# Kernel optimization log

Hardware: AMD Instinct MI355X
Metric: run time of the kernel (lower is better)

The kernel has to match this reference:

```python
import jax, jax.numpy as jnp
import numpy as np

B, HW, ENC = 64, 14, 2048
T_CAP, VOCAB = 25, 10000
EMB = DEC = ATT = 512


def setup_inputs() -> dict:
    key = jax.random.key(0)
    ks = jax.random.split(key, 24)
    n = lambda k, shape, s=0.02: jax.random.normal(k, shape, jnp.float32) * s
    encoder_out = jax.random.normal(ks[0], (B, HW, HW, ENC), jnp.float32)
    captions = jax.random.randint(ks[1], (B, T_CAP), 0, VOCAB)
    lens = jax.random.randint(ks[2], (B,), 2, T_CAP + 1)
    caption_lengths = jnp.sort(lens)[::-1].at[0].set(T_CAP)  # sorted desc, max=T_CAP
    return {
        'encoder_out': encoder_out,
        'captions': captions,
        'caption_lengths': caption_lengths,
        'emb': jax.random.uniform(ks[3], (VOCAB, EMB), jnp.float32, -0.1, 0.1),
        'We_att': n(ks[4], (ENC, ATT)), 'be_att': jnp.zeros((ATT,), jnp.float32),
        'Wd_att': n(ks[5], (DEC, ATT)), 'bd_att': jnp.zeros((ATT,), jnp.float32),
        'v_att': n(ks[6], (ATT, 1)),    'bv_att': jnp.zeros((1,), jnp.float32),
        'W_ih': n(ks[7], (4 * DEC, EMB + ENC)), 'b_ih': jnp.zeros((4 * DEC,), jnp.float32),
        'W_hh': n(ks[8], (4 * DEC, DEC)),       'b_hh': jnp.zeros((4 * DEC,), jnp.float32),
        'W_init_h': n(ks[9], (ENC, DEC)),  'b_init_h': jnp.zeros((DEC,), jnp.float32),
        'W_init_c': n(ks[10], (ENC, DEC)), 'b_init_c': jnp.zeros((DEC,), jnp.float32),
        'W_fbeta': n(ks[11], (DEC, ENC)),  'b_fbeta': jnp.zeros((ENC,), jnp.float32),
        'W_fc': jax.random.uniform(ks[12], (DEC, VOCAB), jnp.float32, -0.1, 0.1),
        'b_fc': jnp.zeros((VOCAB,), jnp.float32),
    }


def reference(encoder_out, captions, caption_lengths, emb,
              We_att, be_att, Wd_att, bd_att, v_att, bv_att,
              W_ih, b_ih, W_hh, b_hh,
              W_init_h, b_init_h, W_init_c, b_init_c,
              W_fbeta, b_fbeta, W_fc, b_fc):
    Bn = encoder_out.shape[0]
    enc = encoder_out.reshape(Bn, -1, encoder_out.shape[-1])  # [B, P=196, ENC]
    decode_lengths = caption_lengths - 1
    T = captions.shape[1] - 1  # static max(decode_lengths)

    emb_cap = emb[captions]                    # [B, T+1, EMB]
    mean_enc = enc.mean(axis=1)                # [B, ENC]
    h0 = mean_enc @ W_init_h + b_init_h        # [B, DEC]
    c0 = mean_enc @ W_init_c + b_init_c
    att1 = enc @ We_att + be_att               # [B, P, ATT], hoisted (same math each step)

    def step(carry, inp):
        h, c = carry
        x_emb, active = inp                    # [B,EMB], [B] bool (batch_size_t mask)
        # attention
        att2 = h @ Wd_att + bd_att             # [B, ATT]
        e = (jax.nn.relu(att1 + att2[:, None, :]) @ v_att)[..., 0] + bv_att[0]  # [B, P]
        alpha = jax.nn.softmax(e, axis=1)
        ctx = jnp.einsum('bp,bpe->be', alpha, enc)
        # gated context
        ctx = jax.nn.sigmoid(h @ W_fbeta + b_fbeta) * ctx
        # LSTMCell (torch gate order i, f, g, o)
        x = jnp.concatenate([x_emb, ctx], axis=1)
        g = x @ W_ih.T + b_ih + h @ W_hh.T + b_hh
        i_g, f_g, g_g, o_g = jnp.split(g, 4, axis=1)
        c_new = jax.nn.sigmoid(f_g) * c + jax.nn.sigmoid(i_g) * jnp.tanh(g_g)
        h_new = jax.nn.sigmoid(o_g) * jnp.tanh(c_new)
        pred = h_new @ W_fc + b_fc             # dropout = identity (eval)
        m = active[:, None]
        pred = jnp.where(m, pred, 0.0)         # padded rows stay zero (as in torch)
        alpha = jnp.where(m, alpha, 0.0)
        h = jnp.where(m, h_new, h)
        c = jnp.where(m, c_new, c)
        return (h, c), (pred, alpha)

    active_ts = jnp.arange(T)[:, None] < decode_lengths[None, :]   # [T, B]
    xs = (jnp.swapaxes(emb_cap[:, :T], 0, 1), active_ts)
    _, (preds, alphas) = jax.lax.scan(step, (h0, c0), xs)
    predictions = jnp.swapaxes(preds, 0, 1)    # [B, T, VOCAB]
    alphas = jnp.swapaxes(alphas, 0, 1)        # [B, T, P]
    return predictions, captions, decode_lengths, alphas
```

## Files before the change

### kernel.cpp

```cpp
#include <hip/hip_runtime.h>
#include <hip/hip_bf16.h>

#define BATCH 64
#define NPIX 196
#define ENCD 2048
#define ATTD 512
#define DECD 512
#define EMBD 512
#define NVOCAB 10000
#define TSTEPS 24
#define KX 3072
#define NPAD 10112

typedef short bf16x8 __attribute__((ext_vector_type(8)));
typedef float f32x4 __attribute__((ext_vector_type(4)));

__device__ inline ushort f2bf(float f) {
    union { float f; unsigned u; } v; v.f = f;
    unsigned r = (v.u + 0x7fff + ((v.u >> 16) & 1)) >> 16;
    return (ushort)r;
}
__device__ inline float bf2f(ushort u) {
    union { unsigned u; float f; } v; v.u = ((unsigned)u) << 16;
    return v.f;
}

__global__ __launch_bounds__(256) void k_prep(
        const float* __restrict__ Wih, const float* __restrict__ Whh,
        const float* __restrict__ Wd, const float* __restrict__ Wfb,
        const float* __restrict__ Wfc, const float* __restrict__ We,
        const float* __restrict__ emb, const int* __restrict__ caps,
        const int* __restrict__ lens,
        ushort* __restrict__ WTj, ushort* __restrict__ BpreT,
        ushort* __restrict__ WfcT, ushort* __restrict__ WeT,
        ushort* __restrict__ embpartb, float* __restrict__ hcacc,
        float* __restrict__ cap_out, float* __restrict__ len_out) {
    __shared__ float tile[64][65];
    int blk = blockIdx.x, tid = threadIdx.x;
    int tx = tid & 63, ty = tid >> 6;
    if (blk < 2048) {
        int j = blk;
        for (int k = 512 + tid; k < KX; k += 256) {
            float v = (k < 2560) ? Wih[(size_t)j * 2560 + k] : Whh[(size_t)j * 512 + (k - 2560)];
            WTj[(size_t)j * KX + k] = f2bf(v);
        }
        if (blk == 0) {
            for (int i = tid; i < 1664; i += 256) {
                if (i < 1600) cap_out[i] = (float)caps[i];
                else          len_out[i - 1600] = (float)(lens[i - 1600] - 1);
            }
        }
    } else if (blk < 2368) {
        int i = blk - 2048;
        int nb = (i % 40) * 64, kb = (i / 40) * 64;
        for (int s = 0; s < 64; s += 4) {
            int k = kb + ty + s, n = nb + tx;
            float v = (n < ATTD) ? Wd[(size_t)k * ATTD + n] : Wfb[(size_t)k * ENCD + (n - ATTD)];
            tile[ty + s][tx] = v;
        }
        __syncthreads();
        for (int s = 0; s < 64; s += 4)
            BpreT[(size_t)(nb + ty + s) * 512 + kb + tx] = f2bf(tile[tx][ty + s]);
    } else if (blk < 3632) {
        int i = blk - 2368;
        int nb = (i % 158) * 64, kb = (i / 158) * 64;
        for (int s = 0; s < 64; s += 4) {
            int k = kb + ty + s, n = nb + tx;
            float v = (n < NVOCAB) ? Wfc[(size_t)k * NVOCAB + n] : 0.f;
            tile[ty + s][tx] = v;
        }
        __syncthreads();
        for (int s = 0; s < 64; s += 4)
            WfcT[(size_t)(nb + ty + s) * 512 + kb + tx] = f2bf(tile[tx][ty + s]);
    } else if (blk < 3888) {
        int i = blk - 3632;
        int nb = (i % 8) * 64, kb = (i / 8) * 64;
        for (int s = 0; s < 64; s += 4) {
            int k = kb + ty + s, n = nb + tx;
            tile[ty + s][tx] = We[(size_t)k * ATTD + n];
        }
        __syncthreads();
        for (int s = 0; s < 64; s += 4)
            WeT[(size_t)(nb + ty + s) * ENCD + kb + tx] = f2bf(tile[tx][ty + s]);
    } else if (blk < 4656) {
        int i = blk - 3888;
        int r0 = (i % 24) * 64;
        int n0 = (i / 24) * 64;
        int w = tid >> 6, l = tid & 63;
        int m = l & 15, kg = l >> 4;
        int n = n0 + w * 16 + m;
        const float* Bp = Wih + (size_t)n * 2560 + kg * 8;
        int tok[4];
#pragma unroll
        for (int mf = 0; mf < 4; ++mf) {
            int row = r0 + m + mf * 16;
            tok[mf] = caps[(row & 63) * 25 + (row >> 6)];
        }
        f32x4 acc[4] = {};
        for (int k0 = 0; k0 < 512; k0 += 32) {
            float4 b0 = *(const float4*)(Bp + k0);
            float4 b1 = *(const float4*)(Bp + k0 + 4);
            bf16x8 bb;
            bb[0] = f2bf(b0.x); bb[1] = f2bf(b0.y); bb[2] = f2bf(b0.z); bb[3] = f2bf(b0.w);
            bb[4] = f2bf(b1.x); bb[5] = f2bf(b1.y); bb[6] = f2bf(b1.z); bb[7] = f2bf(b1.w);
#pragma unroll
            for (int mf = 0; mf < 4; ++mf) {
                const float* ap = emb + (size_t)tok[mf] * 512 + kg * 8 + k0;
                float4 f0 = *(const float4*)ap;
                float4 f1 = *(const float4*)(ap + 4);
                bf16x8 a;
                a[0] = f2bf(f0.x); a[1] = f2bf(f0.y); a[2] = f2bf(f0.z); a[3] = f2bf(f0.w);
                a[4] = f2bf(f1.x); a[5] = f2bf(f1.y); a[6] = f2bf(f1.z); a[7] = f2bf(f1.w);
                acc[mf] = __builtin_amdgcn_mfma_f32_16x16x32_bf16(a, bb, acc[mf], 0, 0, 0);
            }
        }
#pragma unroll
        for (int mf = 0; mf < 4; ++mf)
#pragma unroll
            for (int r = 0; r < 4; ++r)
                embpartb[(size_t)(r0 + mf * 16 + kg * 4 + r) * 2048 + n] = f2bf(acc[mf][r]);
    } else {
        int i = blk - 4656;
        for (int j = tid; j < 2048; j += 256) hcacc[(size_t)i * 2048 + j] = 0.f;
    }
}

__global__ void k_encconv(const float* __restrict__ enc, ushort* __restrict__ encb) {
    size_t i = ((size_t)blockIdx.x * 256 + threadIdx.x) * 8;
    float4 f0 = *(const float4*)(enc + i);
    float4 f1 = *(const float4*)(enc + i + 4);
    union { bf16x8 v; ushort u[8]; } o;
    o.u[0] = f2bf(f0.x); o.u[1] = f2bf(f0.y); o.u[2] = f2bf(f0.z); o.u[3] = f2bf(f0.w);
    o.u[4] = f2bf(f1.x); o.u[5] = f2bf(f1.y); o.u[6] = f2bf(f1.z); o.u[7] = f2bf(f1.w);
    *(bf16x8*)(encb + i) = o.v;
}

__global__ __launch_bounds__(256) void k_meanb(const ushort* __restrict__ encb,
                                               ushort* __restrict__ meanb) {
    int b = blockIdx.x, half = blockIdx.y;
    int e0 = half * 1024 + threadIdx.x * 4;
    const ushort* ep = encb + (size_t)b * NPIX * ENCD + e0;
    float s0 = 0.f, s1 = 0.f, s2 = 0.f, s3 = 0.f;
#pragma unroll 4
    for (int p = 0; p < NPIX; ++p) {
        ushort4 v = *(const ushort4*)(ep + (size_t)p * ENCD);
        s0 += bf2f(v.x); s1 += bf2f(v.y); s2 += bf2f(v.z); s3 += bf2f(v.w);
    }
    const float sc = 1.0f / NPIX;
    ushort4 o;
    o.x = f2bf(s0 * sc); o.y = f2bf(s1 * sc); o.z = f2bf(s2 * sc); o.w = f2bf(s3 * sc);
    *(ushort4*)(meanb + (size_t)b * ENCD + e0) = o;
}

__global__ __launch_bounds__(256) void k_initp(
        const ushort* __restrict__ meanb,
        const float* __restrict__ Wh, const float* __restrict__ Wc,
        float* __restrict__ hcacc) {
    __shared__ float mm[4][256];
    int bg = blockIdx.x * 4;
    int jy = blockIdx.y;
    int kz = blockIdx.z;
    int tid = threadIdx.x;
    for (int i = tid; i < 1024; i += 256) {
        int qq = i >> 8, k = i & 255;
        mm[qq][k] = bf2f(meanb[(size_t)(bg + qq) * ENCD + kz * 256 + k]);
    }
    __syncthreads();
    int j = jy * 256 + tid;
    const float* W; int col;
    if (j < 512) { W = Wh; col = j; } else { W = Wc; col = j - 512; }
    W += (size_t)(kz * 256) * 512 + col;
    float acc[4] = {};
    for (int k = 0; k < 256; ++k) {
        float w = W[(size_t)k * 512];
#pragma unroll
        for (int qq = 0; qq < 4; ++qq) acc[qq] += mm[qq][k] * w;
    }
#pragma unroll
    for (int qq = 0; qq < 4; ++qq)
        atomicAdd(hcacc + (size_t)(bg + qq) * 1024 + j, acc[qq]);
}

__global__ __launch_bounds__(256) void k_initfin(
        const float* __restrict__ hcacc, const float* __restrict__ bh,
        const float* __restrict__ bc, ushort* __restrict__ hbf,
        float* __restrict__ c) {
    int base = blockIdx.x * 2048;
    for (int i = threadIdx.x; i < 2048; i += 256) {
        int idx = base + i;
        int b = idx >> 10, n = idx & 1023;
        float v = hcacc[idx];
        if (n < 512) hbf[(size_t)b * 512 + n] = f2bf(v + bh[n]);
        else         c[(size_t)b * 512 + (n - 512)] = v + bc[n - 512];
    }
}

__global__ __launch_bounds__(256) void k_att1(
        const ushort* __restrict__ encb, const ushort* __restrict__ WeT,
        const float* __restrict__ be, ushort* __restrict__ att1b) {
    int bid = blockIdx.x;
    int L = (bid & 7) * 49 + (bid >> 3);
    int mt = L >> 2, nt = L & 3;
    int w = threadIdx.x >> 6, l = threadIdx.x & 63;
    int wr = w >> 1, wc = w & 1;
    int m0 = mt * 128 + wr * 64;
    int n0 = nt * 128 + wc * 64;
    int ml = l & 15, kg = l >> 4;
    const ushort* aBase = encb + (size_t)(m0 + ml) * ENCD + kg * 8;
    const ushort* bBase = WeT + (size_t)(n0 + ml) * ENCD + kg * 8;
    f32x4 acc[4][4] = {};
    for (int k0 = 0; k0 < ENCD; k0 += 32) {
        bf16x8 bfr[4], afr[4];
#pragma unroll
        for (int nf = 0; nf < 4; ++nf)
            bfr[nf] = *(const bf16x8*)(bBase + (size_t)nf * 16 * ENCD + k0);
#pragma unroll
        for (int mf = 0; mf < 4; ++mf)
            afr[mf] = *(const bf16x8*)(aBase + (size_t)mf * 16 * ENCD + k0);
#pragma unroll
        for (int mf = 0; mf < 4; ++mf)
#pragma unroll
            for (int nf = 0; nf < 4; ++nf)
                acc[mf][nf] = __builtin_amdgcn_mfma_f32_16x16x32_bf16(afr[mf], bfr[nf], acc[mf][nf], 0, 0, 0);
    }
#pragma unroll
    for (int mf = 0; mf < 4; ++mf)
#pragma unroll
        for (int nf = 0; nf < 4; ++nf) {
            int col = n0 + nf * 16 + ml;
            float bias = be[col];
#pragma unroll
            for (int r = 0; r < 4; ++r) {
                int row = m0 + mf * 16 + kg * 4 + r;
                att1b[(size_t)row * ATTD + col] = f2bf(acc[mf][nf][r] + bias);
            }
        }
}

__global__ __launch_bounds__(512) void k_hsmall2(
        const ushort* __restrict__ hb_cur, const ushort* __restrict__ BpreT,
        const float* __restrict__ bd, const float* __restrict__ bfb,
        float* __restrict__ att2, ushort* __restrict__ gateb) {
    __shared__ float part[2][64][68];
    int blk = blockIdx.x;
    int tid = threadIdx.x;
    int w = tid >> 6, l = tid & 63;
    int wq = w & 3, kh = w >> 2;
    int m = l & 15, kg = l >> 4;
    int n = blk * 64 + wq * 16 + m;
    const ushort* B = BpreT + (size_t)n * 512 + kh * 256 + kg * 8;
    const ushort* A = hb_cur + (size_t)m * 512 + kh * 256 + kg * 8;
    f32x4 acc[4] = {};
#pragma unroll
    for (int k0 = 0; k0 < 256; k0 += 32) {
        bf16x8 bfr = *(const bf16x8*)(B + k0);
#pragma unroll
        for (int mf = 0; mf < 4; ++mf) {
            bf16x8 afr = *(const bf16x8*)(A + mf * 16 * 512 + k0);
            acc[mf] = __builtin_amdgcn_mfma_f32_16x16x32_bf16(afr, bfr, acc[mf], 0, 0, 0);
        }
    }
#pragma unroll
    for (int mf = 0; mf < 4; ++mf)
#pragma unroll
        for (int r = 0; r < 4; ++r)
            part[kh][mf * 16 + kg * 4 + r][wq * 16 + m] = acc[mf][r];
    __syncthreads();
    for (int idx = tid; idx < 4096; idx += 512) {
        int b = idx >> 6, nn = idx & 63;
        float v = part[0][b][nn] + part[1][b][nn];
        int ng = blk * 64 + nn;
        if (ng < 512) att2[(size_t)b * 512 + ng] = v + bd[ng];
        else {
            int e = ng - 512;
            gateb[(size_t)b * 2048 + e] = f2bf(1.f / (1.f + __expf(-(v + bfb[e]))));
        }
    }
}

__global__ __launch_bounds__(512) void k_scorectx(
        const ushort* __restrict__ att1b, const float* __restrict__ att2,
        const float* __restrict__ vatt, const float* __restrict__ bv,
        const ushort* __restrict__ gateb, const int* __restrict__ lens,
        const ushort* __restrict__ encb,
        ushort* __restrict__ ctxb, float* __restrict__ alpha_out, int t) {
    __shared__ float ev[200];
    __shared__ float cpart[4][512];
    __shared__ float inv_s;
    int bid = blockIdx.x;
    int b = ((bid & 7) << 3) | ((bid >> 3) & 7);
    int q = bid >> 6;
    int tid = threadIdx.x;
    int w = tid >> 6, l = tid & 63;
    if (t >= lens[b] - 1) {
        if (q == 0 && tid < NPIX)
            alpha_out[((size_t)b * TSTEPS + t) * NPIX + tid] = 0.f;
        return;
    }
    {
        float a2r[8], vvr[8];
        const float* att2b = att2 + (size_t)b * ATTD;
#pragma unroll
        for (int i = 0; i < 8; ++i) {
            a2r[i] = att2b[l * 8 + i];
            vvr[i] = vatt[l * 8 + i];
        }
        float bv0 = bv[0];
        for (int pp = w; pp < NPIX; pp += 8) {
            bf16x8 f = *(const bf16x8*)(att1b + ((size_t)b * NPIX + pp) * ATTD + l * 8);
            float s = 0.f;
#pragma unroll
            for (int i = 0; i < 8; ++i)
                s += fmaxf(bf2f((ushort)f[i]) + a2r[i], 0.f) * vvr[i];
            for (int off = 32; off > 0; off >>= 1) s += __shfl_down(s, off);
            if (l == 0) ev[pp] = s + bv0;
        }
    }
    __syncthreads();
    if (w == 0) {
        float mx = -1e30f;
        for (int pp = l; pp < NPIX; pp += 64) mx = fmaxf(mx, ev[pp]);
        for (int off = 32; off > 0; off >>= 1) mx = fmaxf(mx, __shfl_down(mx, off));
        mx = __shfl(mx, 0);
        float s = 0.f;
        for (int pp = l; pp < NPIX; pp += 64) {
            float e_ = __expf(ev[pp] - mx);
            ev[pp] = e_;
            s += e_;
        }
        for (int off = 32; off > 0; off >>= 1) s += __shfl_down(s, off);
        if (l == 0) inv_s = 1.0f / s;
    }
    __syncthreads();
    float inv = inv_s;
    if (q == 0 && tid < NPIX)
        alpha_out[((size_t)b * TSTEPS + t) * NPIX + tid] = ev[tid] * inv;
    {
        int pg = tid >> 7, th = tid & 127;
        const ushort* ep = encb + (size_t)b * NPIX * ENCD + q * 512 + th * 4;
        float s0 = 0.f, s1 = 0.f, s2 = 0.f, s3 = 0.f;
        for (int pp = pg; pp < NPIX; pp += 4) {
            ushort4 v = *(const ushort4*)(ep + (size_t)pp * ENCD);
            float al = ev[pp];
            s0 += al * bf2f(v.x); s1 += al * bf2f(v.y);
            s2 += al * bf2f(v.z); s3 += al * bf2f(v.w);
        }
        cpart[pg][th * 4 + 0] = s0;
        cpart[pg][th * 4 + 1] = s1;
        cpart[pg][th * 4 + 2] = s2;
        cpart[pg][th * 4 + 3] = s3;
    }
    __syncthreads();
    if (tid < 128) {
        ushort4 g4 = *(const ushort4*)(gateb + (size_t)b * 2048 + q * 512 + tid * 4);
        ushort4 o;
        o.x = f2bf((cpart[0][tid * 4 + 0] + cpart[1][tid * 4 + 0] + cpart[2][tid * 4 + 0] + cpart[3][tid * 4 + 0]) * inv * bf2f(g4.x));
        o.y = f2bf((cpart[0][tid * 4 + 1] + cpart[1][tid * 4 + 1] + cpart[2][tid * 4 + 1] + cpart[3][tid * 4 + 1]) * inv * bf2f(g4.y));
        o.z = f2bf((cpart[0][tid * 4 + 2] + cpart[1][tid * 4 + 2] + cpart[2][tid * 4 + 2] + cpart[3][tid * 4 + 2]) * inv * bf2f(g4.z));
        o.w = f2bf((cpart[0][tid * 4 + 3] + cpart[1][tid * 4 + 3] + cpart[2][tid * 4 + 3] + cpart[3][tid * 4 + 3]) * inv * bf2f(g4.w));
        *(ushort4*)(ctxb + (size_t)b * 2048 + q * 512 + tid * 4) = o;
    }
}

__global__ __launch_bounds__(512) void k_gates2(
        const ushort* __restrict__ ctxb, const ushort* __restrict__ hb_cur,
        const ushort* __restrict__ WTj, const ushort* __restrict__ embpartb,
        const float* __restrict__ bih, const float* __restrict__ bhh,
        const int* __restrict__ lens, float* __restrict__ c,
        ushort* __restrict__ hb_nxt, ushort* __restrict__ hAll, int t) {
    __shared__ float part[8][64][16];
    int g = blockIdx.x;
    int tid = threadIdx.x;
    int w = tid >> 6, l = tid & 63;
    int m = l & 15, kg = l >> 4;
    int jrow = (m >> 2) * 512 + g * 4 + (m & 3);
    const ushort* Brow = WTj + (size_t)jrow * KX;
    f32x4 acc[4] = {};
    {
        const ushort* B = Brow + 512 + w * 256 + kg * 8;
        const ushort* A = ctxb + (size_t)m * 2048 + w * 256 + kg * 8;
#pragma unroll
        for (int k0 = 0; k0 < 256; k0 += 32) {
            bf16x8 bfr = *(const bf16x8*)(B + k0);
#pragma unroll
            for (int mf = 0; mf < 4; ++mf) {
                bf16x8 afr = *(const bf16x8*)(A + (size_t)mf * 16 * 2048 + k0);
                acc[mf] = __builtin_amdgcn_mfma_f32_16x16x32_bf16(afr, bfr, acc[mf], 0, 0, 0);
            }
        }
    }
    {
        const ushort* B = Brow + 2560 + w * 64 + kg * 8;
        const ushort* A = hb_cur + (size_t)m * 512 + w * 64 + kg * 8;
#pragma unroll
        for (int k0 = 0; k0 < 64; k0 += 32) {
            bf16x8 bfr = *(const bf16x8*)(B + k0);
#pragma unroll
            for (int mf = 0; mf < 4; ++mf) {
                bf16x8 afr = *(const bf16x8*)(A + (size_t)mf * 16 * 512 + k0);
                acc[mf] = __builtin_amdgcn_mfma_f32_16x16x32_bf16(afr, bfr, acc[mf], 0, 0, 0);
            }
        }
    }
#pragma unroll
    for (int mf = 0; mf < 4; ++mf)
#pragma unroll
        for (int r = 0; r < 4; ++r)
            part[w][mf * 16 + kg * 4 + r][m] = acc[mf][r];
    __syncthreads();
    if (tid < 256) {
        int bb = tid >> 2, j = tid & 3;
        int d = g * 4 + j;
        float gi = 0.f, gf = 0.f, gg = 0.f, go = 0.f;
#pragma unroll
        for (int w8 = 0; w8 < 8; ++w8) {
            gi += part[w8][bb][j];
            gf += part[w8][bb][4 + j];
            gg += part[w8][bb][8 + j];
            go += part[w8][bb][12 + j];
        }
        ushort hout = hb_cur[(size_t)bb * 512 + d];
        if (t < lens[bb] - 1) {
            const ushort* eb = embpartb + ((size_t)t * 64 + bb) * 2048;
            gi += bf2f(eb[d])        + bih[d]        + bhh[d];
            gf += bf2f(eb[512 + d])  + bih[512 + d]  + bhh[512 + d];
            gg += bf2f(eb[1024 + d]) + bih[1024 + d] + bhh[1024 + d];
            go += bf2f(eb[1536 + d]) + bih[1536 + d] + bhh[1536 + d];
            float cc = c[(size_t)bb * 512 + d];
            float si = 1.f / (1.f + __expf(-gi));
            float sf = 1.f / (1.f + __expf(-gf));
            float so = 1.f / (1.f + __expf(-go));
            float cn = sf * cc + si * tanhf(gg);
            float hn = so * tanhf(cn);
            c[(size_t)bb * 512 + d] = cn;
            hout = f2bf(hn);
        }
        hb_nxt[(size_t)bb * 512 + d] = hout;
        hAll[((size_t)t * 64 + bb) * 512 + d] = hout;
    }
}

__global__ __launch_bounds__(256) void k_predall(
        const ushort* __restrict__ hAll, const ushort* __restrict__ WfcT,
        const float* __restrict__ bfc, const int* __restrict__ lens,
        float* __restrict__ pred) {
    int w = threadIdx.x >> 6, l = threadIdx.x & 63;
    int wr = w >> 1, wc = w & 1;
    int m0 = blockIdx.x * 128 + wr * 64;
    int n0 = blockIdx.y * 128 + wc * 64;
    int ml = l & 15, kg = l >> 4;
    const ushort* aBase = hAll + (size_t)(m0 + ml) * 512 + kg * 8;
    const ushort* bBase = WfcT + (size_t)(n0 + ml) * 512 + kg * 8;
    f32x4 acc[4][4] = {};
#pragma unroll 2
    for (int k0 = 0; k0 < 512; k0 += 32) {
        bf16x8 bfr[4], afr[4];
#pragma unroll
        for (int nf = 0; nf < 4; ++nf)
            bfr[nf] = *(const bf16x8*)(bBase + (size_t)nf * 16 * 512 + k0);
#pragma unroll
        for (int mf = 0; mf < 4; ++mf)
            afr[mf] = *(const bf16x8*)(aBase + (size_t)mf * 16 * 512 + k0);
#pragma unroll
        for (int mf = 0; mf < 4; ++mf)
#pragma unroll
            for (int nf = 0; nf < 4; ++nf)
                acc[mf][nf] = __builtin_amdgcn_mfma_f32_16x16x32_bf16(afr[mf], bfr[nf], acc[mf][nf], 0, 0, 0);
    }
#pragma unroll
    for (int mf = 0; mf < 4; ++mf)
#pragma unroll
        for (int nf = 0; nf < 4; ++nf) {
            int col = n0 + nf * 16 + ml;
            if (col < NVOCAB) {
                float bias = bfc[col];
#pragma unroll
                for (int r = 0; r < 4; ++r) {
                    int row = m0 + mf * 16 + kg * 4 + r;
                    int t = row >> 6, b = row & 63;
                    bool act = t < (lens[b] - 1);
                    pred[((size_t)b * TSTEPS + t) * NVOCAB + col] = act ? acc[mf][nf][r] + bias : 0.f;
                }
            }
        }
}

extern "C" void kernel_launch(void* const* d_in, const int* in_sizes, int n_in,
                              void* d_out, int out_size, void* d_ws, size_t ws_size,
                              hipStream_t stream) {
    const float* enc  = (const float*)d_in[0];
    const int*   caps = (const int*)d_in[1];
    const int*   lens = (const int*)d_in[2];
    const float* emb  = (const float*)d_in[3];
    const float* We   = (const float*)d_in[4];
    const float* be   = (const float*)d_in[5];
    const float* Wd   = (const float*)d_in[6];
    const float* bd   = (const float*)d_in[7];
    const float* vatt = (const float*)d_in[8];
    const float* bv   = (const float*)d_in[9];
    const float* Wih  = (const float*)d_in[10];
    const float* bih  = (const float*)d_in[11];
    const float* Whh  = (const float*)d_in[12];
    const float* bhh  = (const float*)d_in[13];
    const float* Winh = (const float*)d_in[14];
    const float* binh = (const float*)d_in[15];
    const float* Winc = (const float*)d_in[16];
    const float* binc = (const float*)d_in[17];
    const float* Wfb  = (const float*)d_in[18];
    const float* bfb  = (const float*)d_in[19];
    const float* Wfc  = (const float*)d_in[20];
    const float* bfc  = (const float*)d_in[21];

    float* out       = (float*)d_out;
    float* pred_out  = out;
    float* cap_out   = out + 15360000;
    float* len_out   = out + 15361600;
    float* alpha_out = out + 15361664;

    char* p = (char*)d_ws;
    ushort* att1b    = (ushort*)p; p += (size_t)12544 * 512 * 2;
    ushort* WTj      = (ushort*)p; p += (size_t)2048 * KX * 2;
    ushort* WfcT     = (ushort*)p; p += (size_t)NPAD * 512 * 2;
    ushort* BpreT    = (ushort*)p; p += (size_t)2560 * 512 * 2;
    ushort* WeT      = (ushort*)p; p += (size_t)512 * 2048 * 2;
    ushort* embpartb = (ushort*)p; p += (size_t)1536 * 2048 * 2;
    ushort* hAll     = (ushort*)p; p += (size_t)1536 * 512 * 2;
    ushort* ctxb     = (ushort*)p; p += (size_t)64 * 2048 * 2;
    ushort* hb0      = (ushort*)p; p += (size_t)64 * 512 * 2;
    ushort* hb1      = (ushort*)p; p += (size_t)64 * 512 * 2;
    float* c         = (float*)p;  p += (size_t)64 * 512 * 4;
    ushort* meanb    = (ushort*)p; p += (size_t)64 * 2048 * 2;
    float* att2      = (float*)p;  p += (size_t)64 * 512 * 4;
    ushort* gateb    = (ushort*)p; p += (size_t)64 * 2048 * 2;
    ushort* encb     = (ushort*)p; p += (size_t)64 * NPIX * ENCD * 2;
    float* hcacc     = (float*)ctxb;

    k_prep<<<4688, 256, 0, stream>>>(Wih, Whh, Wd, Wfb, Wfc, We, emb, caps, lens,
                                     WTj, BpreT, WfcT, WeT, embpartb, hcacc,
                                     cap_out, len_out);
    k_encconv<<<12544, 256, 0, stream>>>(enc, encb);
    k_meanb<<<dim3(64, 2), 256, 0, stream>>>(encb, meanb);
    k_initp<<<dim3(16, 4, 8), 256, 0, stream>>>(meanb, Winh, Winc, hcacc);
    k_initfin<<<32, 256, 0, stream>>>(hcacc, binh, binc, hb0, c);
    k_att1<<<392, 256, 0, stream>>>(encb, WeT, be, att1b);

    for (int t = 0; t < TSTEPS; ++t) {
        const ushort* hcur = (t & 1) ? hb1 : hb0;
        ushort* hnxt = (t & 1) ? hb0 : hb1;
        k_hsmall2<<<40, 512, 0, stream>>>(hcur, BpreT, bd, bfb, att2, gateb);
        k_scorectx<<<256, 512, 0, stream>>>(att1b, att2, vatt, bv, gateb, lens,
                                            encb, ctxb, alpha_out, t);
        k_gates2<<<128, 512, 0, stream>>>(ctxb, hcur, WTj, embpartb, bih, bhh,
                                          lens, c, hnxt, hAll, t);
    }
    k_predall<<<dim3(12, 79), 256, 0, stream>>>(hAll, WfcT, bfc, lens, pred_out);
}
```

Before: 1.785 ms.

## Split att1 GEMM K across two wave groups and vectorize prep transposes

The att1 GEMM kernel now launches 512 threads per block. The two halves of the waves each handle half of the 2048-long K dimension, and their partial accumulators are summed through a ~66KB shared-memory buffer before the bias is added and the result stored. This doubles the waves available to hide latency for the 392-block launch, at the cost of LDS use and a block-wide barrier that may reduce occupancy. Separately, the weight-transpose sections of the prep kernel now read float4 instead of scalar floats to cut global load instructions.

```diff
diff --git a/kernel.cpp b/kernel.cpp
--- a/kernel.cpp
+++ b/kernel.cpp
@@ -38,6 +38,7 @@
     __shared__ float tile[64][65];
     int blk = blockIdx.x, tid = threadIdx.x;
     int tx = tid & 63, ty = tid >> 6;
+    int fx = tid & 15, fy = tid >> 4;
     if (blk < 2048) {
         int j = blk;
         for (int k = 512 + tid; k < KX; k += 256) {
@@ -53,10 +54,15 @@
     } else if (blk < 2368) {
         int i = blk - 2048;
         int nb = (i % 40) * 64, kb = (i / 40) * 64;
-        for (int s = 0; s < 64; s += 4) {
-            int k = kb + ty + s, n = nb + tx;
-            float v = (n < ATTD) ? Wd[(size_t)k * ATTD + n] : Wfb[(size_t)k * ENCD + (n - ATTD)];
-            tile[ty + s][tx] = v;
+        for (int s = 0; s < 4; ++s) {
+            int k = kb + fy + s * 16;
+            int n = nb + fx * 4;
+            float4 v = (n < ATTD) ? *(const float4*)(Wd + (size_t)k * ATTD + n)
+                                  : *(const float4*)(Wfb + (size_t)k * ENCD + (n - ATTD));
+            tile[fy + s * 16][fx * 4 + 0] = v.x;
+            tile[fy + s * 16][fx * 4 + 1] = v.y;
+            tile[fy + s * 16][fx * 4 + 2] = v.z;
+            tile[fy + s * 16][fx * 4 + 3] = v.w;
         }
         __syncthreads();
         for (int s = 0; s < 64; s += 4)
@@ -64,10 +70,15 @@
     } else if (blk < 3632) {
         int i = blk - 2368;
         int nb = (i % 158) * 64, kb = (i / 158) * 64;
-        for (int s = 0; s < 64; s += 4) {
-            int k = kb + ty + s, n = nb + tx;
-            float v = (n < NVOCAB) ? Wfc[(size_t)k * NVOCAB + n] : 0.f;
-            tile[ty + s][tx] = v;
+        for (int s = 0; s < 4; ++s) {
+            int k = kb + fy + s * 16;
+            int n = nb + fx * 4;
+            float4 v = make_float4(0.f, 0.f, 0.f, 0.f);
+            if (n < NVOCAB) v = *(const float4*)(Wfc + (size_t)k * NVOCAB + n);
+            tile[fy + s * 16][fx * 4 + 0] = v.x;
+            tile[fy + s * 16][fx * 4 + 1] = v.y;
+            tile[fy + s * 16][fx * 4 + 2] = v.z;
+            tile[fy + s * 16][fx * 4 + 3] = v.w;
         }
         __syncthreads();
         for (int s = 0; s < 64; s += 4)
@@ -75,9 +86,14 @@
     } else if (blk < 3888) {
         int i = blk - 3632;
         int nb = (i % 8) * 64, kb = (i / 8) * 64;
-        for (int s = 0; s < 64; s += 4) {
-            int k = kb + ty + s, n = nb + tx;
-            tile[ty + s][tx] = We[(size_t)k * ATTD + n];
+        for (int s = 0; s < 4; ++s) {
+            int k = kb + fy + s * 16;
+            int n = nb + fx * 4;
+            float4 v = *(const float4*)(We + (size_t)k * ATTD + n);
+            tile[fy + s * 16][fx * 4 + 0] = v.x;
+            tile[fy + s * 16][fx * 4 + 1] = v.y;
+            tile[fy + s * 16][fx * 4 + 2] = v.z;
+            tile[fy + s * 16][fx * 4 + 3] = v.w;
         }
         __syncthreads();
         for (int s = 0; s < 64; s += 4)
@@ -195,21 +211,24 @@
     }
 }
 
-__global__ __launch_bounds__(256) void k_att1(
+__global__ __launch_bounds__(512) void k_att1(
         const ushort* __restrict__ encb, const ushort* __restrict__ WeT,
         const float* __restrict__ be, ushort* __restrict__ att1b) {
+    __shared__ float red[4][64][65];
     int bid = blockIdx.x;
     int L = (bid & 7) * 49 + (bid >> 3);
     int mt = L >> 2, nt = L & 3;
-    int w = threadIdx.x >> 6, l = threadIdx.x & 63;
-    int wr = w >> 1, wc = w & 1;
+    int tid = threadIdx.x;
+    int w = tid >> 6, l = tid & 63;
+    int q = w & 3, kh = w >> 2;
+    int wr = q >> 1, wc = q & 1;
     int m0 = mt * 128 + wr * 64;
     int n0 = nt * 128 + wc * 64;
     int ml = l & 15, kg = l >> 4;
-    const ushort* aBase = encb + (size_t)(m0 + ml) * ENCD + kg * 8;
-    const ushort* bBase = WeT + (size_t)(n0 + ml) * ENCD + kg * 8;
+    const ushort* aBase = encb + (size_t)(m0 + ml) * ENCD + kh * 1024 + kg * 8;
+    const ushort* bBase = WeT + (size_t)(n0 + ml) * ENCD + kh * 1024 + kg * 8;
     f32x4 acc[4][4] = {};
-    for (int k0 = 0; k0 < ENCD; k0 += 32) {
+    for (int k0 = 0; k0 < 1024; k0 += 32) {
         bf16x8 bfr[4], afr[4];
 #pragma unroll
         for (int nf = 0; nf < 4; ++nf)
@@ -223,18 +242,31 @@
             for (int nf = 0; nf < 4; ++nf)
                 acc[mf][nf] = __builtin_amdgcn_mfma_f32_16x16x32_bf16(afr[mf], bfr[nf], acc[mf][nf], 0, 0, 0);
     }
-#pragma unroll
-    for (int mf = 0; mf < 4; ++mf)
-#pragma unroll
-        for (int nf = 0; nf < 4; ++nf) {
-            int col = n0 + nf * 16 + ml;
-            float bias = be[col];
-#pragma unroll
-            for (int r = 0; r < 4; ++r) {
-                int row = m0 + mf * 16 + kg * 4 + r;
-                att1b[(size_t)row * ATTD + col] = f2bf(acc[mf][nf][r] + bias);
+    if (kh == 1) {
+#pragma unroll
+        for (int mf = 0; mf < 4; ++mf)
+#pragma unroll
+            for (int nf = 0; nf < 4; ++nf)
+#pragma unroll
+                for (int r = 0; r < 4; ++r)
+                    red[q][mf * 16 + kg * 4 + r][nf * 16 + ml] = acc[mf][nf][r];
+    }
+    __syncthreads();
+    if (kh == 0) {
+#pragma unroll
+        for (int mf = 0; mf < 4; ++mf)
+#pragma unroll
+            for (int nf = 0; nf < 4; ++nf) {
+                int col = n0 + nf * 16 + ml;
+                float bias = be[col];
+#pragma unroll
+                for (int r = 0; r < 4; ++r) {
+                    int row = m0 + mf * 16 + kg * 4 + r;
+                    float v = acc[mf][nf][r] + red[q][mf * 16 + kg * 4 + r][nf * 16 + ml];
+                    att1b[(size_t)row * ATTD + col] = f2bf(v + bias);
+                }
             }
-        }
+    }
 }
 
 __global__ __launch_bounds__(512) void k_hsmall2(
@@ -542,7 +574,7 @@
     k_meanb<<<dim3(64, 2), 256, 0, stream>>>(encb, meanb);
     k_initp<<<dim3(16, 4, 8), 256, 0, stream>>>(meanb, Winh, Winc, hcacc);
     k_initfin<<<32, 256, 0, stream>>>(hcacc, binh, binc, hb0, c);
-    k_att1<<<392, 256, 0, stream>>>(encb, WeT, be, att1b);
+    k_att1<<<392, 512, 0, stream>>>(encb, WeT, be, att1b);
 
     for (int t = 0; t < TSTEPS; ++t) {
         const ushort* hcur = (t & 1) ? hb1 : hb0;
```

Measured after the change: 1.778 ms. No clear change (-0.4%).
